# Performance work log

Hardware: AMD Instinct MI355X
Metric: run time of the kernel (lower is better)

## Reference

```python
import jax, jax.numpy as jnp
import numpy as np

HEAD_SIZE = 64
HEADS = 12

def _rope(x):
    # x: [B, L, d]; bert4torch interleaved RoPE: q*cos + rotate_every_two(q)*sin
    L, d = x.shape[-2], x.shape[-1]
    inv_freq = 1.0 / (10000.0 ** (jnp.arange(0, d, 2, dtype=jnp.float32) / d))
    ang = jnp.arange(L, dtype=jnp.float32)[:, None] * inv_freq  # [L, d/2]
    sin = jnp.repeat(jnp.sin(ang), 2, axis=-1)  # [L, d]
    cos = jnp.repeat(jnp.cos(ang), 2, axis=-1)  # [L, d]
    x2 = jnp.stack([-x[..., 1::2], x[..., ::2]], axis=-1).reshape(x.shape)
    return x * cos + x2 * sin

def setup_inputs() -> dict:
    key = jax.random.key(0)
    ks = jax.random.split(key, 4)
    B, L, H = 2, 2048, 1024
    inputs = jax.random.normal(ks[0], (B, L, H), dtype=jnp.float32)
    mask = jnp.ones((B, L), dtype=jnp.int32)
    Wp = jax.random.normal(ks[1], (H, 2 * HEAD_SIZE), dtype=jnp.float32) * (1.0 / np.sqrt(H))
    bp = jnp.zeros((2 * HEAD_SIZE,), dtype=jnp.float32)
    Wq = jax.random.normal(ks[2], (2 * HEAD_SIZE, 2 * HEADS), dtype=jnp.float32) * (1.0 / np.sqrt(2 * HEAD_SIZE))
    bq = jnp.zeros((2 * HEADS,), dtype=jnp.float32)
    return {"inputs": inputs, "mask": mask, "Wp": Wp, "bp": bp, "Wq": Wq, "bq": bq}

def reference(inputs, mask, Wp, bp, Wq, bq):
    B, L, _ = inputs.shape
    seq_out = inputs @ Wp + bp                          # [B, L, 2*hs]
    qw, kw = seq_out[..., :HEAD_SIZE], seq_out[..., HEAD_SIZE:]
    qw, kw = _rope(qw), _rope(kw)
    scores = jnp.einsum('bmd,bnd->bmn', qw, kw) / jnp.sqrt(jnp.float32(HEAD_SIZE))  # [B, L, L]
    # chunk(heads, -1) + stack(-2) == reshape(B, L, heads, 2); transpose(1,2) -> [B, H, L, 2]
    bias = (seq_out @ Wq + bq).reshape(B, L, HEADS, 2) / 2.0
    bias = jnp.transpose(bias, (0, 2, 1, 3))            # [B, H, L, 2]
    logits = scores[:, None] + bias[..., :1] + jnp.swapaxes(bias[..., 1:], 2, 3)  # [B, H, L, L]
    m = mask.astype(bool)
    neg_inf = jnp.float32(-jnp.inf)
    logits = jnp.where(m[:, None, :, None], logits, neg_inf)
    logits = jnp.where(m[:, None, None, :], logits, neg_inf)
    tril = jnp.tril(jnp.ones((L, L), dtype=logits.dtype), -1)
    logits = logits - tril * jnp.float32(1e12)
    return logits
```

## Files before the change

### kernel.cpp

```cpp
#include <hip/hip_runtime.h>
#include <math.h>

#define LSEQ 2048
#define NB 2
#define HDIM 1024
#define NKV 128
#define MALL (NB*LSEQ)

__global__ __launch_bounds__(256) void k1_gemm(const float* __restrict__ A,
                                               const float* __restrict__ Wp,
                                               float* __restrict__ Cp) {
    const int nt    = blockIdx.x & 1;
    const int split = blockIdx.x >> 1;
    const int m0 = blockIdx.y * 64;
    const int n0 = nt * 64;
    __shared__ float As[32][68];
    __shared__ float Bs[32][64];
    const int tid = threadIdx.x;
    const int tm = tid & 15;
    const int tn = tid >> 4;
    float acc[4][4] = {};
    for (int kc = 0; kc < 16; ++kc) {
        const int k0 = split*512 + kc*32;
        #pragma unroll
        for (int p = 0; p < 2; ++p) {
            int idx = tid + 256*p;
            int row = idx >> 3, kq = idx & 7;
            float4 a = *(const float4*)(A + (size_t)(m0+row)*HDIM + k0 + 4*kq);
            As[4*kq+0][row] = a.x;
            As[4*kq+1][row] = a.y;
            As[4*kq+2][row] = a.z;
            As[4*kq+3][row] = a.w;
        }
        #pragma unroll
        for (int p = 0; p < 2; ++p) {
            int idx = tid + 256*p;
            int r = idx >> 4, c = idx & 15;
            *(float4*)(&Bs[r][4*c]) = *(const float4*)(Wp + (size_t)(k0+r)*NKV + n0 + 4*c);
        }
        __syncthreads();
        #pragma unroll
        for (int kk = 0; kk < 32; ++kk) {
            float4 av = *(const float4*)(&As[kk][4*tm]);
            float4 bv = *(const float4*)(&Bs[kk][4*tn]);
            float aa[4] = {av.x, av.y, av.z, av.w};
            float bb[4] = {bv.x, bv.y, bv.z, bv.w};
            #pragma unroll
            for (int i = 0; i < 4; ++i)
                #pragma unroll
                for (int j = 0; j < 4; ++j)
                    acc[i][j] = fmaf(aa[i], bb[j], acc[i][j]);
        }
        __syncthreads();
    }
    float* outp = Cp + (size_t)split*MALL*NKV;
    #pragma unroll
    for (int i = 0; i < 4; ++i) {
        float4 v = make_float4(acc[i][0], acc[i][1], acc[i][2], acc[i][3]);
        *(float4*)(outp + (size_t)(m0 + 4*tm + i)*NKV + n0 + 4*tn) = v;
    }
}

__global__ __launch_bounds__(64) void k2_rope_bias(const float* __restrict__ Cp,
        const float* __restrict__ bp, const float* __restrict__ Wq,
        const float* __restrict__ bq, float* __restrict__ qwout,
        float* __restrict__ kwout, float* __restrict__ biasQ,
        float* __restrict__ biasK) {
    const int row = blockIdx.x;
    const int b = row >> 11;
    const int l = row & (LSEQ - 1);
    const int t = threadIdx.x;
    const float* r0 = Cp + (size_t)row*NKV;
    const float* r1 = r0 + (size_t)MALL*NKV;
    float x0 = r0[2*t]   + r1[2*t]   + bp[2*t];
    float x1 = r0[2*t+1] + r1[2*t+1] + bp[2*t+1];
    const int p = t & 31;
    float inv = exp2f(-0.41524101186098287f * (float)p);
    float ang = (float)l * inv;
    float sn = sinf(ang), cs = cosf(ang);
    float y0 = x0*cs - x1*sn;
    float y1 = x1*cs + x0*sn;
    float* dst = (t < 32) ? (qwout + (size_t)row*64) : (kwout + (size_t)row*64);
    dst[2*p]   = y0;
    dst[2*p+1] = y1;
    float res = 0.f;
    for (int j = 0; j < 24; ++j) {
        float part = fmaf(x0, Wq[(2*t)*24 + j], x1 * Wq[(2*t+1)*24 + j]);
        #pragma unroll
        for (int off = 32; off > 0; off >>= 1)
            part += __shfl_xor(part, off);
        if (t == j) res = part;
    }
    if (t < 24) {
        float v = (res + bq[t]) * 0.5f;
        int h = t >> 1;
        float* bb = (t & 1) ? biasK : biasQ;
        bb[((size_t)b*12 + h)*LSEQ + l] = v;
    }
}

__global__ __launch_bounds__(256) void k3_scores(const float* __restrict__ qw,
        const float* __restrict__ kwv, const float* __restrict__ biasQ,
        const float* __restrict__ biasK, const int* __restrict__ mask,
        float* __restrict__ out) {
    const int n0 = blockIdx.x * 64;
    const int m0 = blockIdx.y * 32;
    const int b  = blockIdx.z;
    const int tid = threadIdx.x;
    const int tn = tid & 63;
    const int tm = tid >> 6;
    __shared__ float qlds[32*64];
    __shared__ float bQ[12][32];
    __shared__ float bK[12][64];
    __shared__ float mM[32];
    __shared__ float mN[64];
    const size_t rowbase = (size_t)b * LSEQ;
    #pragma unroll
    for (int pld = 0; pld < 2; ++pld) {
        int idx = tid + 256*pld;
        int r = idx >> 4, q = idx & 15;
        *(float4*)&qlds[r*64 + 4*q] =
            *(const float4*)(qw + (rowbase + m0 + r)*64 + 4*q);
    }
    for (int i = tid; i < 384; i += 256) {
        int h = i >> 5, m = i & 31;
        bQ[h][m] = biasQ[((size_t)b*12 + h)*LSEQ + m0 + m];
    }
    for (int i = tid; i < 768; i += 256) {
        int h = i >> 6, n = i & 63;
        bK[h][n] = biasK[((size_t)b*12 + h)*LSEQ + n0 + n];
    }
    if (tid < 32)       mM[tid]    = (mask[rowbase + m0 + tid] != 0) ? 1.f : 0.f;
    else if (tid < 96)  mN[tid-32] = (mask[rowbase + n0 + (tid-32)] != 0) ? 1.f : 0.f;
    float4 kr[16];
    const float4* kp = (const float4*)(kwv + (rowbase + n0 + tn)*64);
    #pragma unroll
    for (int j = 0; j < 16; ++j) kr[j] = kp[j];
    __syncthreads();

    const float4* q4 = (const float4*)qlds;
    float accv[8];
    #pragma unroll
    for (int i = 0; i < 8; ++i) {
        const int ml = tm*8 + i;
        float s = 0.f;
        #pragma unroll
        for (int j = 0; j < 16; ++j) {
            float4 qv = q4[ml*16 + j];
            s = fmaf(qv.x, kr[j].x, s);
            s = fmaf(qv.y, kr[j].y, s);
            s = fmaf(qv.z, kr[j].z, s);
            s = fmaf(qv.w, kr[j].w, s);
        }
        accv[i] = s * 0.125f;
    }
    const int n = n0 + tn;
    const float mn = mN[tn];
    float bk[12];
    #pragma unroll
    for (int h = 0; h < 12; ++h) bk[h] = bK[h][tn];
    #pragma unroll
    for (int i = 0; i < 8; ++i) {
        const int ml = tm*8 + i;
        const int m = m0 + ml;
        const float pen = (m > n) ? 1e12f : 0.f;
        const bool ok = (mM[ml] != 0.f) && (mn != 0.f);
        size_t off = (size_t)b*12*LSEQ*LSEQ + (size_t)m*LSEQ + n;
        #pragma unroll
        for (int h = 0; h < 12; ++h) {
            float v = accv[i] + bQ[h][ml] + bk[h];
            v = ok ? v : -INFINITY;
            v -= pen;
            out[off + (size_t)h*LSEQ*LSEQ] = v;
        }
    }
}

extern "C" void kernel_launch(void* const* d_in, const int* in_sizes, int n_in,
                              void* d_out, int out_size, void* d_ws, size_t ws_size,
                              hipStream_t stream) {
    const float* inputs = (const float*)d_in[0];
    const int*   mask   = (const int*)  d_in[1];
    const float* Wp     = (const float*)d_in[2];
    const float* bp     = (const float*)d_in[3];
    const float* Wq     = (const float*)d_in[4];
    const float* bq     = (const float*)d_in[5];
    float* out = (float*)d_out;

    float* Cp  = (float*)d_ws;
    float* qwb = Cp  + (size_t)2*MALL*NKV;
    float* kwb = qwb + (size_t)MALL*64;
    float* bQ  = kwb + (size_t)MALL*64;
    float* bK  = bQ  + (size_t)NB*12*LSEQ;

    k1_gemm     <<<dim3(4, 64),     256, 0, stream>>>(inputs, Wp, Cp);
    k2_rope_bias<<<dim3(MALL),       64, 0, stream>>>(Cp, bp, Wq, bq, qwb, kwb, bQ, bK);
    k3_scores   <<<dim3(32, 64, 2), 256, 0, stream>>>(qwb, kwb, bQ, bK, mask, out);
}
```

Baseline: 467.9 us.

## Restructure scores kernel to per-row-pair blocks with streaming stores; split GEMM K four ways

```diff
diff --git a/kernel.cpp b/kernel.cpp
--- a/kernel.cpp
+++ b/kernel.cpp
@@ -6,6 +6,7 @@
 #define HDIM 1024
 #define NKV 128
 #define MALL (NB*LSEQ)
+#define KSPLIT 4
 
 __global__ __launch_bounds__(256) void k1_gemm(const float* __restrict__ A,
                                                const float* __restrict__ Wp,
@@ -20,8 +21,8 @@
     const int tm = tid & 15;
     const int tn = tid >> 4;
     float acc[4][4] = {};
-    for (int kc = 0; kc < 16; ++kc) {
-        const int k0 = split*512 + kc*32;
+    for (int kc = 0; kc < 8; ++kc) {
+        const int k0 = split*256 + kc*32;
         #pragma unroll
         for (int p = 0; p < 2; ++p) {
             int idx = tid + 256*p;
@@ -70,10 +71,13 @@
     const int b = row >> 11;
     const int l = row & (LSEQ - 1);
     const int t = threadIdx.x;
-    const float* r0 = Cp + (size_t)row*NKV;
-    const float* r1 = r0 + (size_t)MALL*NKV;
-    float x0 = r0[2*t]   + r1[2*t]   + bp[2*t];
-    float x1 = r0[2*t+1] + r1[2*t+1] + bp[2*t+1];
+    float x0 = bp[2*t], x1 = bp[2*t+1];
+    #pragma unroll
+    for (int s = 0; s < KSPLIT; ++s) {
+        const float* r = Cp + (size_t)s*MALL*NKV + (size_t)row*NKV;
+        x0 += r[2*t];
+        x1 += r[2*t+1];
+    }
     const int p = t & 31;
     float inv = exp2f(-0.41524101186098287f * (float)p);
     float ang = (float)l * inv;
@@ -99,79 +103,86 @@
     }
 }
 
-__global__ __launch_bounds__(256) void k3_scores(const float* __restrict__ qw,
+__global__ __launch_bounds__(256, 2) void k3_scores(const float* __restrict__ qw,
         const float* __restrict__ kwv, const float* __restrict__ biasQ,
         const float* __restrict__ biasK, const int* __restrict__ mask,
         float* __restrict__ out) {
-    const int n0 = blockIdx.x * 64;
-    const int m0 = blockIdx.y * 32;
-    const int b  = blockIdx.z;
+    const int m0 = blockIdx.x * 4;
+    const int b  = blockIdx.y;
     const int tid = threadIdx.x;
-    const int tn = tid & 63;
-    const int tm = tid >> 6;
-    __shared__ float qlds[32*64];
-    __shared__ float bQ[12][32];
-    __shared__ float bK[12][64];
-    __shared__ float mM[32];
-    __shared__ float mN[64];
+    const int nl = tid & 127;
+    const int g  = tid >> 7;
+    __shared__ float kws[128 * 68];
+
     const size_t rowbase = (size_t)b * LSEQ;
+    const int mA = m0 + 2*g, mB = mA + 1;
+
+    float4 q0[16], q1[16];
+    {
+        const float4* qp0 = (const float4*)(qw + (rowbase + mA)*64);
+        const float4* qp1 = (const float4*)(qw + (rowbase + mB)*64);
+        #pragma unroll
+        for (int j = 0; j < 16; ++j) { q0[j] = qp0[j]; q1[j] = qp1[j]; }
+    }
+    float bq0[12], bq1[12];
     #pragma unroll
-    for (int pld = 0; pld < 2; ++pld) {
-        int idx = tid + 256*pld;
-        int r = idx >> 4, q = idx & 15;
-        *(float4*)&qlds[r*64 + 4*q] =
-            *(const float4*)(qw + (rowbase + m0 + r)*64 + 4*q);
-    }
-    for (int i = tid; i < 384; i += 256) {
-        int h = i >> 5, m = i & 31;
-        bQ[h][m] = biasQ[((size_t)b*12 + h)*LSEQ + m0 + m];
-    }
-    for (int i = tid; i < 768; i += 256) {
-        int h = i >> 6, n = i & 63;
-        bK[h][n] = biasK[((size_t)b*12 + h)*LSEQ + n0 + n];
-    }
-    if (tid < 32)       mM[tid]    = (mask[rowbase + m0 + tid] != 0) ? 1.f : 0.f;
-    else if (tid < 96)  mN[tid-32] = (mask[rowbase + n0 + (tid-32)] != 0) ? 1.f : 0.f;
-    float4 kr[16];
-    const float4* kp = (const float4*)(kwv + (rowbase + n0 + tn)*64);
-    #pragma unroll
-    for (int j = 0; j < 16; ++j) kr[j] = kp[j];
-    __syncthreads();
-
-    const float4* q4 = (const float4*)qlds;
-    float accv[8];
-    #pragma unroll
-    for (int i = 0; i < 8; ++i) {
-        const int ml = tm*8 + i;
-        float s = 0.f;
+    for (int h = 0; h < 12; ++h) {
+        const float* bqp = biasQ + ((size_t)b*12 + h)*LSEQ;
+        bq0[h] = bqp[mA];
+        bq1[h] = bqp[mB];
+    }
+    const bool okmA = mask[rowbase + mA] != 0;
+    const bool okmB = mask[rowbase + mB] != 0;
+    const size_t outbase = (size_t)b * 12 * LSEQ * LSEQ;
+
+    for (int c = 0; c < 16; ++c) {
+        const int nbase = c * 128;
+        __syncthreads();
+        #pragma unroll
+        for (int p = 0; p < 8; ++p) {
+            int f4 = tid + 256*p;
+            int r = f4 >> 4, q16 = f4 & 15;
+            float4 v = *(const float4*)(kwv + (rowbase + nbase + r)*64 + 4*q16);
+            *(float4*)(&kws[r*68 + 4*q16]) = v;
+        }
+        __syncthreads();
+
+        const int n = nbase + nl;
+        float acc0 = 0.f, acc1 = 0.f;
+        const float4* kr = (const float4*)(&kws[nl * 68]);
         #pragma unroll
         for (int j = 0; j < 16; ++j) {
-            float4 qv = q4[ml*16 + j];
-            s = fmaf(qv.x, kr[j].x, s);
-            s = fmaf(qv.y, kr[j].y, s);
-            s = fmaf(qv.z, kr[j].z, s);
-            s = fmaf(qv.w, kr[j].w, s);
-        }
-        accv[i] = s * 0.125f;
-    }
-    const int n = n0 + tn;
-    const float mn = mN[tn];
-    float bk[12];
-    #pragma unroll
-    for (int h = 0; h < 12; ++h) bk[h] = bK[h][tn];
-    #pragma unroll
-    for (int i = 0; i < 8; ++i) {
-        const int ml = tm*8 + i;
-        const int m = m0 + ml;
-        const float pen = (m > n) ? 1e12f : 0.f;
-        const bool ok = (mM[ml] != 0.f) && (mn != 0.f);
-        size_t off = (size_t)b*12*LSEQ*LSEQ + (size_t)m*LSEQ + n;
+            float4 kv = kr[j];
+            acc0 = fmaf(q0[j].x, kv.x, acc0);
+            acc0 = fmaf(q0[j].y, kv.y, acc0);
+            acc0 = fmaf(q0[j].z, kv.z, acc0);
+            acc0 = fmaf(q0[j].w, kv.w, acc0);
+            acc1 = fmaf(q1[j].x, kv.x, acc1);
+            acc1 = fmaf(q1[j].y, kv.y, acc1);
+            acc1 = fmaf(q1[j].z, kv.z, acc1);
+            acc1 = fmaf(q1[j].w, kv.w, acc1);
+        }
+        acc0 *= 0.125f;
+        acc1 *= 0.125f;
+
+        const bool okn = mask[rowbase + n] != 0;
+        const float penA = (mA > n) ? 1e12f : 0.f;
+        const float penB = (mB > n) ? 1e12f : 0.f;
+        const bool okA = okmA && okn;
+        const bool okB = okmB && okn;
+        size_t offA = outbase + (size_t)mA * LSEQ + n;
+        const float* bkp = biasK + (size_t)b*12*LSEQ + n;
         #pragma unroll
         for (int h = 0; h < 12; ++h) {
-            float v = accv[i] + bQ[h][ml] + bk[h];
-            v = ok ? v : -INFINITY;
-            v -= pen;
-            out[off + (size_t)h*LSEQ*LSEQ] = v;
+            float bk = bkp[(size_t)h * LSEQ];
+            float v0 = acc0 + bq0[h] + bk;
+            v0 = okA ? v0 : -INFINITY;
+            v0 -= penA;
+            float v1 = acc1 + bq1[h] + bk;
+            v1 = okB ? v1 : -INFINITY;
+            v1 -= penB;
+            __builtin_nontemporal_store(v0, &out[offA + (size_t)h*LSEQ*LSEQ]);
+            __builtin_nontemporal_store(v1, &out[offA + LSEQ + (size_t)h*LSEQ*LSEQ]);
         }
     }
 }
@@ -188,12 +199,12 @@
     float* out = (float*)d_out;
 
     float* Cp  = (float*)d_ws;
-    float* qwb = Cp  + (size_t)2*MALL*NKV;
+    float* qwb = Cp  + (size_t)KSPLIT*MALL*NKV;
     float* kwb = qwb + (size_t)MALL*64;
     float* bQ  = kwb + (size_t)MALL*64;
     float* bK  = bQ  + (size_t)NB*12*LSEQ;
 
-    k1_gemm     <<<dim3(4, 64),     256, 0, stream>>>(inputs, Wp, Cp);
-    k2_rope_bias<<<dim3(MALL),       64, 0, stream>>>(Cp, bp, Wq, bq, qwb, kwb, bQ, bK);
-    k3_scores   <<<dim3(32, 64, 2), 256, 0, stream>>>(qwb, kwb, bQ, bK, mask, out);
-}
+    k1_gemm     <<<dim3(8, 64),   256, 0, stream>>>(inputs, Wp, Cp);
+    k2_rope_bias<<<dim3(MALL),     64, 0, stream>>>(Cp, bp, Wq, bq, qwb, kwb, bQ, bK);
+    k3_scores   <<<dim3(512, 2), 256, 0, stream>>>(qwb, kwb, bQ, bK, mask, out);
+}
```

After: 465.9 us. No clear change (-0.4%).
